# Kernel optimization log

Measured on AMD Instinct MI355X. Metric: run time of the kernel, lower is better.

Reference implementation:

```python
import jax, jax.numpy as jnp
import numpy as np

B, T, F, U = 256, 1024, 64, 128  # batch, history_size, model_input_num, GRU units


def gru(x_seq, W, Uk, b, return_sequences):
    """Keras GRU (reset_after=True, recurrent_activation=sigmoid, activation=relu).
    x_seq: [B,T,F_in]; W: [F_in,3U]; Uk: [U,3U]; b: [2,3U] (input bias, recurrent bias).
    """
    b_i, b_r = b[0], b[1]
    xw = jnp.einsum('bti,iu->btu', x_seq, W) + b_i  # precompute input projection [B,T,3U]

    def step(h, xw_t):
        rec = h @ Uk + b_r                          # [B,3U]
        xz, xr, xh = jnp.split(xw_t, 3, axis=-1)
        rz, rr, rh = jnp.split(rec, 3, axis=-1)
        z = jax.nn.sigmoid(xz + rz)
        r = jax.nn.sigmoid(xr + rr)
        hh = jax.nn.relu(xh + r * rh)
        h_new = z * h + (1.0 - z) * hh
        return h_new, h_new

    h0 = jnp.zeros((x_seq.shape[0], Uk.shape[0]), dtype=x_seq.dtype)
    hT, hs = jax.lax.scan(step, h0, jnp.swapaxes(xw, 0, 1))  # scan over time
    if return_sequences:
        return jnp.swapaxes(hs, 0, 1), hT  # [B,T,U], [B,U]
    return hT, hT


def setup_inputs() -> dict:
    key = jax.random.key(0)
    ks = jax.random.split(key, 7)
    s_in1 = 1.0 / np.sqrt(F)
    s_rec = 1.0 / np.sqrt(U)
    return {
        'input_data': jax.random.normal(ks[0], (B, T, F), dtype=jnp.float32),
        'W1': jax.random.normal(ks[1], (F, 3 * U), dtype=jnp.float32) * s_in1,
        'U1': jax.random.normal(ks[2], (U, 3 * U), dtype=jnp.float32) * s_rec,
        'b1': jnp.zeros((2, 3 * U), dtype=jnp.float32),
        'W2': jax.random.normal(ks[3], (U, 3 * U), dtype=jnp.float32) * s_rec,
        'U2': jax.random.normal(ks[4], (U, 3 * U), dtype=jnp.float32) * s_rec,
        'b2': jnp.zeros((2, 3 * U), dtype=jnp.float32),
    }


def reference(input_data, W1, U1, b1, W2, U2, b2):
    seq1, state1 = gru(input_data, W1, U1, b1, return_sequences=True)
    x, state2 = gru(seq1, W2, U2, b2, return_sequences=False)
    return (x, state1, state2)
```

## Files before the change

### kernel.cpp

```cpp
#include <hip/hip_runtime.h>


#define TT 1024
#define FF 64
#define G3 384
#define NB 16
#define CHUNK 32
#define NCH (TT / CHUNK)
#define FLAG_BYTES ((size_t)NB * NCH * 4)
#define H1F_BYTES ((size_t)NB * TT * 4096)
#define PIPE_WS (FLAG_BYTES + H1F_BYTES)

typedef __attribute__((ext_vector_type(8))) __bf16 bf16x8;
typedef __attribute__((ext_vector_type(4))) float f32x4;

#define MFMA(a, b, c) __builtin_amdgcn_mfma_f32_16x16x32_bf16((a), (b), (c), 0, 0, 0)

__device__ __forceinline__ float sigf(float x) {
    return __builtin_amdgcn_rcpf(1.0f + __expf(-x));
}

__device__ __forceinline__ void wait_flag(const unsigned int* f) {
    while (__hip_atomic_load(f, __ATOMIC_ACQUIRE, __HIP_MEMORY_SCOPE_AGENT) == 0u)
        __builtin_amdgcn_s_sleep(1);
}

__global__ __launch_bounds__(512)
__attribute__((amdgpu_waves_per_eu(2, 2)))
void gru_pipe2(
    const float* __restrict__ x,  const float* __restrict__ W1,
    const float* __restrict__ U1, const float* __restrict__ b1,
    const float* __restrict__ W2, const float* __restrict__ U2,
    const float* __restrict__ b2, unsigned char* __restrict__ ws,
    float* __restrict__ out)
{
    const int tid  = threadIdx.x;
    const int wave = tid >> 6;
    const int lane = tid & 63;
    const int quad = lane >> 4;
    const int lc   = lane & 15;
    const int rb   = blockIdx.x & 15;
    const int row0 = rb * 16;
    const int u    = wave * 16 + lc;

    unsigned int* flags = (unsigned int*)ws + rb * NCH;
    unsigned char* h1f  = ws + FLAG_BYTES + (size_t)rb * TT * 4096;

    __shared__ __align__(16) __bf16 hs[2][16][140];
    for (int i = tid; i < 2 * 16 * 140; i += 512)
        ((__bf16*)hs)[i] = (__bf16)0.f;

    const f32x4 zeroq = {0.f, 0.f, 0.f, 0.f};

    if (blockIdx.x < NB) {
        bf16x8 U1B[3][4], W1B[3][2];
#pragma unroll
        for (int g = 0; g < 3; g++) {
#pragma unroll
            for (int kt = 0; kt < 4; kt++) {
                bf16x8 a;
#pragma unroll
                for (int j = 0; j < 8; j++)
                    a[j] = (__bf16)U1[(kt * 32 + quad * 8 + j) * G3 + g * 128 + u];
                U1B[g][kt] = a;
            }
#pragma unroll
            for (int kt = 0; kt < 2; kt++) {
                bf16x8 a;
#pragma unroll
                for (int j = 0; j < 8; j++)
                    a[j] = (__bf16)W1[(kt * 32 + quad * 8 + j) * G3 + g * 128 + u];
                W1B[g][kt] = a;
            }
        }
        const float c1z  = b1[u] + b1[G3 + u];
        const float c1r  = b1[128 + u] + b1[G3 + 128 + u];
        const float b1ih = b1[256 + u];
        const float b1rh = b1[G3 + 256 + u];
        const f32x4 c1zq  = {c1z, c1z, c1z, c1z};
        const f32x4 c1rq  = {c1r, c1r, c1r, c1r};
        const f32x4 b1ihq = {b1ih, b1ih, b1ih, b1ih};
        const f32x4 b1rhq = {b1rh, b1rh, b1rh, b1rh};

        const float* xrow = x + (size_t)(row0 + lc) * (TT * FF) + quad * 8;
        f32x4 xp0 = *(const f32x4*)(xrow);
        f32x4 xp1 = *(const f32x4*)(xrow + 4);
        f32x4 xp2 = *(const f32x4*)(xrow + 32);
        f32x4 xp3 = *(const f32x4*)(xrow + 36);

        float h1c[4] = {0, 0, 0, 0};
        __syncthreads();

#define PSTEP(T, PAR)                                                          \
    {                                                                          \
        bf16x8 A1[4];                                                          \
        _Pragma("unroll") for (int kt = 0; kt < 4; kt++)                       \
            A1[kt] = *(const bf16x8*)&hs[PAR ^ 1][lc][kt * 32 + quad * 8];     \
        bf16x8 xa0, xa1;                                                       \
        _Pragma("unroll") for (int j = 0; j < 4; j++) {                        \
            xa0[j] = (__bf16)xp0[j]; xa0[j + 4] = (__bf16)xp1[j];              \
            xa1[j] = (__bf16)xp2[j]; xa1[j + 4] = (__bf16)xp3[j];              \
        }                                                                      \
        if ((T) + 1 < TT) {                                                    \
            const float* px = xrow + (size_t)((T) + 1) * FF;                   \
            xp0 = *(const f32x4*)px;                                           \
            xp1 = *(const f32x4*)(px + 4);                                     \
            xp2 = *(const f32x4*)(px + 32);                                    \
            xp3 = *(const f32x4*)(px + 36);                                    \
        }                                                                      \
                    \
        f32x4 z1a = MFMA(xa0, W1B[0][0], c1zq);                                \
        f32x4 r1a = MFMA(xa0, W1B[1][0], c1rq);                                \
        f32x4 xh1 = MFMA(xa0, W1B[2][0], b1ihq);                               \
        z1a = MFMA(xa1, W1B[0][1], z1a);                                       \
        r1a = MFMA(xa1, W1B[1][1], r1a);                                       \
        xh1 = MFMA(xa1, W1B[2][1], xh1);                                       \
                                     \
        f32x4 z1b = MFMA(A1[0], U1B[0][0], zeroq);                             \
        f32x4 r1b = MFMA(A1[0], U1B[1][0], zeroq);                             \
        f32x4 rh1 = MFMA(A1[0], U1B[2][0], b1rhq);                             \
        f32x4 z1d = MFMA(A1[1], U1B[0][1], zeroq);                             \
        f32x4 r1d = MFMA(A1[1], U1B[1][1], zeroq);                             \
        rh1 = MFMA(A1[1], U1B[2][1], rh1);                                     \
        z1b = MFMA(A1[2], U1B[0][2], z1b);                                     \
        r1b = MFMA(A1[2], U1B[1][2], r1b);                                     \
        rh1 = MFMA(A1[2], U1B[2][2], rh1);                                     \
        z1d = MFMA(A1[3], U1B[0][3], z1d);                                     \
        r1d = MFMA(A1[3], U1B[1][3], r1d);                                     \
        rh1 = MFMA(A1[3], U1B[2][3], rh1);                                     \
        if ((T) > 0 && wave == 0) {        \
            _Pragma("unroll") for (int kt = 0; kt < 4; kt++)                   \
                *(bf16x8*)(h1f + ((size_t)((T) - 1) * 4 + kt) * 1024           \
                           + lane * 16) = A1[kt];                              \
        }                                                                      \
        f32x4 z1 = z1a + (z1b + z1d);                                          \
        f32x4 r1 = r1a + (r1b + r1d);                                          \
        _Pragma("unroll") for (int i = 0; i < 4; i++) {                        \
            float zf = sigf(z1[i]);                                            \
            float rf = sigf(r1[i]);                                            \
            float hh = fmaxf(xh1[i] + rf * rh1[i], 0.f);                       \
            h1c[i] = fmaf(zf, h1c[i] - hh, hh);                                \
            hs[PAR][quad * 4 + i][u] = (__bf16)h1c[i];                         \
        }                                                                      \
        if (wave == 0 && (T) > 0 && (((T) & (CHUNK - 1)) == 0)) {              \
            __threadfence();                                                   \
            if (lane == 0)                                                     \
                __hip_atomic_store(flags + ((T) / CHUNK) - 1, 1u,              \
                                   __ATOMIC_RELEASE,                           \
                                   __HIP_MEMORY_SCOPE_AGENT);                  \
        }                                                                      \
        asm volatile("s_waitcnt lgkmcnt(0)\n\ts_barrier" ::: "memory");        \
    }

        for (int t = 0; t < TT; t += 2) {
            PSTEP(t, 0)
            PSTEP(t + 1, 1)
        }
#undef PSTEP

        if (wave == 0) {
#pragma unroll
            for (int kt = 0; kt < 4; kt++) {
                bf16x8 a = *(const bf16x8*)&hs[1][lc][kt * 32 + quad * 8];
                *(bf16x8*)(h1f + ((size_t)(TT - 1) * 4 + kt) * 1024
                           + lane * 16) = a;
            }
            __threadfence();
            if (lane == 0)
                __hip_atomic_store(flags + NCH - 1, 1u, __ATOMIC_RELEASE,
                                   __HIP_MEMORY_SCOPE_AGENT);
        }
#pragma unroll
        for (int i = 0; i < 4; i++) {
            int r = row0 + quad * 4 + i;
            out[32768 + (size_t)r * 128 + u] = h1c[i];
        }
    } else {
        bf16x8 W2B[3][4], U2B[3][4];
#pragma unroll
        for (int g = 0; g < 3; g++)
#pragma unroll
            for (int kt = 0; kt < 4; kt++) {
                bf16x8 b, c;
#pragma unroll
                for (int j = 0; j < 8; j++) {
                    int k = (kt * 32 + quad * 8 + j) * G3 + g * 128 + u;
                    b[j] = (__bf16)W2[k];
                    c[j] = (__bf16)U2[k];
                }
                W2B[g][kt] = b;
                U2B[g][kt] = c;
            }
        const float c2z  = b2[u] + b2[G3 + u];
        const float c2r  = b2[128 + u] + b2[G3 + 128 + u];
        const float b2ih = b2[256 + u];
        const float b2rh = b2[G3 + 256 + u];
        const f32x4 c2zq  = {c2z, c2z, c2z, c2z};
        const f32x4 c2rq  = {c2r, c2r, c2r, c2r};
        const f32x4 b2ihq = {b2ih, b2ih, b2ih, b2ih};
        const f32x4 b2rhq = {b2rh, b2rh, b2rh, b2rh};

        float h2c[4] = {0, 0, 0, 0};
        bf16x8 hAa0, hAa1, hAa2, hAa3, hAb0, hAb1, hAb2, hAb3;
        __syncthreads();

#define CSTEP(T, PAR, C0, C1, C2, C3)                                          \
    {                                                                          \
        bf16x8 A2[4];                                                          \
        _Pragma("unroll") for (int kt = 0; kt < 4; kt++)                       \
            A2[kt] = *(const bf16x8*)&hs[PAR ^ 1][lc][kt * 32 + quad * 8];     \
                    \
        f32x4 z2a = MFMA(C0, W2B[0][0], c2zq);                                 \
        f32x4 r2a = MFMA(C0, W2B[1][0], c2rq);                                 \
        f32x4 xh2 = MFMA(C0, W2B[2][0], b2ihq);                                \
        f32x4 z2c = MFMA(C1, W2B[0][1], zeroq);                                \
        f32x4 r2c = MFMA(C1, W2B[1][1], zeroq);                                \
        xh2 = MFMA(C1, W2B[2][1], xh2);                                        \
        z2a = MFMA(C2, W2B[0][2], z2a);                                        \
        r2a = MFMA(C2, W2B[1][2], r2a);                                        \
        xh2 = MFMA(C2, W2B[2][2], xh2);                                        \
        z2c = MFMA(C3, W2B[0][3], z2c);                                        \
        r2c = MFMA(C3, W2B[1][3], r2c);                                        \
        xh2 = MFMA(C3, W2B[2][3], xh2);                                        \
        if ((T) + 2 < tend) {      \
            const unsigned char* sp =                                          \
                h1f + (size_t)((T) + 2) * 4096 + lane * 16;                    \
            C0 = *(const bf16x8*)(sp);                                         \
            C1 = *(const bf16x8*)(sp + 1024);                                  \
            C2 = *(const bf16x8*)(sp + 2048);                                  \
            C3 = *(const bf16x8*)(sp + 3072);                                  \
        }                                                                      \
                                     \
        f32x4 z2b = MFMA(A2[0], U2B[0][0], zeroq);                             \
        f32x4 r2b = MFMA(A2[0], U2B[1][0], zeroq);                             \
        f32x4 rh2 = MFMA(A2[0], U2B[2][0], b2rhq);                             \
        f32x4 z2d = MFMA(A2[1], U2B[0][1], zeroq);                             \
        f32x4 r2d = MFMA(A2[1], U2B[1][1], zeroq);                             \
        rh2 = MFMA(A2[1], U2B[2][1], rh2);                                     \
        z2b = MFMA(A2[2], U2B[0][2], z2b);                                     \
        r2b = MFMA(A2[2], U2B[1][2], r2b);                                     \
        rh2 = MFMA(A2[2], U2B[2][2], rh2);                                     \
        z2d = MFMA(A2[3], U2B[0][3], z2d);                                     \
        r2d = MFMA(A2[3], U2B[1][3], r2d);                                     \
        rh2 = MFMA(A2[3], U2B[2][3], rh2);                                     \
        f32x4 z2 = (z2a + z2c) + (z2b + z2d);                                  \
        f32x4 r2 = (r2a + r2c) + (r2b + r2d);                                  \
        _Pragma("unroll") for (int i = 0; i < 4; i++) {                        \
            float zf = sigf(z2[i]);                                            \
            float rf = sigf(r2[i]);                                            \
            float hh = fmaxf(xh2[i] + rf * rh2[i], 0.f);                       \
            h2c[i] = fmaf(zf, h2c[i] - hh, hh);                                \
            hs[PAR][quad * 4 + i][u] = (__bf16)h2c[i];                         \
        }                                                                      \
        asm volatile("s_waitcnt lgkmcnt(0)\n\ts_barrier" ::: "memory");        \
    }

        for (int c = 0; c < NCH; c++) {
            wait_flag(flags + c);
            const int t0   = c * CHUNK;
            const int tend = t0 + CHUNK;
            {
                const unsigned char* sp = h1f + (size_t)t0 * 4096 + lane * 16;
                hAa0 = *(const bf16x8*)(sp);
                hAa1 = *(const bf16x8*)(sp + 1024);
                hAa2 = *(const bf16x8*)(sp + 2048);
                hAa3 = *(const bf16x8*)(sp + 3072);
                const unsigned char* sq = sp + 4096;
                hAb0 = *(const bf16x8*)(sq);
                hAb1 = *(const bf16x8*)(sq + 1024);
                hAb2 = *(const bf16x8*)(sq + 2048);
                hAb3 = *(const bf16x8*)(sq + 3072);
            }
            for (int t = t0; t < tend; t += 2) {
                CSTEP(t, 0, hAa0, hAa1, hAa2, hAa3)
                CSTEP(t + 1, 1, hAb0, hAb1, hAb2, hAb3)
            }
        }
#undef CSTEP

#pragma unroll
        for (int i = 0; i < 4; i++) {
            int r = row0 + quad * 4 + i;
            out[(size_t)r * 128 + u]         = h2c[i];
            out[65536 + (size_t)r * 128 + u] = h2c[i];
        }
    }
}

__global__ __launch_bounds__(512)
__attribute__((amdgpu_waves_per_eu(2, 2)))
void gru_mono(
    const float* __restrict__ x,  const float* __restrict__ W1,
    const float* __restrict__ U1, const float* __restrict__ b1,
    const float* __restrict__ W2, const float* __restrict__ U2,
    const float* __restrict__ b2, float* __restrict__ out)
{
    const int tid  = threadIdx.x;
    const int wave = tid >> 6;
    const int lane = tid & 63;
    const int quad = lane >> 4;
    const int lc   = lane & 15;
    const int row0 = blockIdx.x * 16;
    const int u    = wave * 16 + lc;

    __shared__ __align__(16) __bf16 h1s[2][16][136];
    __shared__ __align__(16) __bf16 h2s[2][16][136];
    for (int i = tid; i < 2 * 16 * 136; i += 512) {
        ((__bf16*)h1s)[i] = (__bf16)0.f;
        ((__bf16*)h2s)[i] = (__bf16)0.f;
    }

    bf16x8 U1B[3][4], W2B[3][4], U2B[3][4], W1B[3][2];
#pragma unroll
    for (int g = 0; g < 3; g++) {
#pragma unroll
        for (int kt = 0; kt < 4; kt++) {
            bf16x8 a, b, c;
#pragma unroll
            for (int j = 0; j < 8; j++) {
                int k = (kt * 32 + quad * 8 + j) * G3 + g * 128 + u;
                a[j] = (__bf16)U1[k];
                b[j] = (__bf16)W2[k];
                c[j] = (__bf16)U2[k];
            }
            U1B[g][kt] = a; W2B[g][kt] = b; U2B[g][kt] = c;
        }
#pragma unroll
        for (int kt = 0; kt < 2; kt++) {
            bf16x8 a;
#pragma unroll
            for (int j = 0; j < 8; j++)
                a[j] = (__bf16)W1[(kt * 32 + quad * 8 + j) * G3 + g * 128 + u];
            W1B[g][kt] = a;
        }
    }

    const float c1z  = b1[u] + b1[G3 + u];
    const float c1r  = b1[128 + u] + b1[G3 + 128 + u];
    const float b1ih = b1[256 + u];
    const float b1rh = b1[G3 + 256 + u];
    const float c2z  = b2[u] + b2[G3 + u];
    const float c2r  = b2[128 + u] + b2[G3 + 128 + u];
    const float b2ih = b2[256 + u];
    const float b2rh = b2[G3 + 256 + u];
    const f32x4 c1zq  = {c1z, c1z, c1z, c1z};
    const f32x4 c1rq  = {c1r, c1r, c1r, c1r};
    const f32x4 b1ihq = {b1ih, b1ih, b1ih, b1ih};
    const f32x4 b1rhq = {b1rh, b1rh, b1rh, b1rh};
    const f32x4 c2zq  = {c2z, c2z, c2z, c2z};
    const f32x4 c2rq  = {c2r, c2r, c2r, c2r};
    const f32x4 b2ihq = {b2ih, b2ih, b2ih, b2ih};
    const f32x4 b2rhq = {b2rh, b2rh, b2rh, b2rh};

    const float* xrow = x + (size_t)(row0 + lc) * (TT * FF) + quad * 8;
    float h1c[4] = {0, 0, 0, 0};
    float h2c[4] = {0, 0, 0, 0};
    __syncthreads();

#define MSTEP(T, PAR)                                                          \
    {                                                                          \
        bf16x8 A1[4];                                                          \
        _Pragma("unroll") for (int kt = 0; kt < 4; kt++)                       \
            A1[kt] = *(const bf16x8*)&h1s[PAR ^ 1][lc][kt * 32 + quad * 8];    \
        const float* px = xrow + (size_t)(T) * FF;                             \
        f32x4 u0 = *(const f32x4*)px;                                          \
        f32x4 u1 = *(const f32x4*)(px + 4);                                    \
        f32x4 u2 = *(const f32x4*)(px + 32);                                   \
        f32x4 u3 = *(const f32x4*)(px + 36);                                   \
        bf16x8 xa0, xa1;                                                       \
        _Pragma("unroll") for (int j = 0; j < 4; j++) {                        \
            xa0[j] = (__bf16)u0[j]; xa0[j + 4] = (__bf16)u1[j];                \
            xa1[j] = (__bf16)u2[j]; xa1[j + 4] = (__bf16)u3[j];                \
        }                                                                      \
        f32x4 z1  = MFMA(xa0, W1B[0][0], c1zq);                                \
        z1        = MFMA(xa1, W1B[0][1], z1);                                  \
        f32x4 r1  = MFMA(xa0, W1B[1][0], c1rq);                                \
        r1        = MFMA(xa1, W1B[1][1], r1);                                  \
        f32x4 xh1 = MFMA(xa0, W1B[2][0], b1ihq);                               \
        xh1       = MFMA(xa1, W1B[2][1], xh1);                                 \
        f32x4 rh1 = MFMA(A1[0], U1B[2][0], b1rhq);                             \
        z1        = MFMA(A1[0], U1B[0][0], z1);                                \
        r1        = MFMA(A1[0], U1B[1][0], r1);                                \
        _Pragma("unroll") for (int kt = 1; kt < 4; kt++) {                     \
            z1  = MFMA(A1[kt], U1B[0][kt], z1);                                \
            r1  = MFMA(A1[kt], U1B[1][kt], r1);                                \
            rh1 = MFMA(A1[kt], U1B[2][kt], rh1);                               \
        }                                                                      \
        _Pragma("unroll") for (int i = 0; i < 4; i++) {                        \
            float zf = sigf(z1[i]);                                            \
            float rf = sigf(r1[i]);                                            \
            float hh = fmaxf(xh1[i] + rf * rh1[i], 0.f);                       \
            h1c[i] = fmaf(zf, h1c[i] - hh, hh);                                \
            h1s[PAR][quad * 4 + i][u] = (__bf16)h1c[i];                        \
        }                                                                      \
        f32x4 z2  = MFMA(A1[0], W2B[0][0], c2zq);                              \
        f32x4 r2  = MFMA(A1[0], W2B[1][0], c2rq);                              \
        f32x4 xh2 = MFMA(A1[0], W2B[2][0], b2ihq);                             \
        _Pragma("unroll") for (int kt = 1; kt < 4; kt++) {                     \
            z2  = MFMA(A1[kt], W2B[0][kt], z2);                                \
            r2  = MFMA(A1[kt], W2B[1][kt], r2);                                \
            xh2 = MFMA(A1[kt], W2B[2][kt], xh2);                               \
        }                                                                      \
        f32x4 rh2;                                                             \
        {                                                                      \
            bf16x8 A2 = *(const bf16x8*)&h2s[PAR][lc][quad * 8];               \
            rh2 = MFMA(A2, U2B[2][0], b2rhq);                                  \
            z2  = MFMA(A2, U2B[0][0], z2);                                     \
            r2  = MFMA(A2, U2B[1][0], r2);                                     \
        }                                                                      \
        _Pragma("unroll") for (int kt = 1; kt < 4; kt++) {                     \
            bf16x8 A2 = *(const bf16x8*)&h2s[PAR][lc][kt * 32 + quad * 8];     \
            z2  = MFMA(A2, U2B[0][kt], z2);                                    \
            r2  = MFMA(A2, U2B[1][kt], r2);                                    \
            rh2 = MFMA(A2, U2B[2][kt], rh2);                                   \
        }                                                                      \
        if ((T) > 0) {                                                         \
            _Pragma("unroll") for (int i = 0; i < 4; i++) {                    \
                float zf = sigf(z2[i]);                                        \
                float rf = sigf(r2[i]);                                        \
                float hh = fmaxf(xh2[i] + rf * rh2[i], 0.f);                   \
                h2c[i] = fmaf(zf, h2c[i] - hh, hh);                            \
            }                                                                  \
        }                                                                      \
        _Pragma("unroll") for (int i = 0; i < 4; i++)                          \
            h2s[PAR ^ 1][quad * 4 + i][u] = (__bf16)h2c[i];                    \
        asm volatile("s_waitcnt lgkmcnt(0)\n\ts_barrier" ::: "memory");        \
    }

    for (int t = 0; t < TT; t += 2) {
        MSTEP(t, 0)
        MSTEP(t + 1, 1)
    }
#undef MSTEP

    {
        f32x4 z2 = c2zq, r2 = c2rq, xh2 = b2ihq, rh2 = b2rhq;
#pragma unroll
        for (int kt = 0; kt < 4; kt++) {
            bf16x8 a1 = *(const bf16x8*)&h1s[1][lc][kt * 32 + quad * 8];
            bf16x8 a2 = *(const bf16x8*)&h2s[0][lc][kt * 32 + quad * 8];
            z2  = MFMA(a1, W2B[0][kt], z2);
            r2  = MFMA(a1, W2B[1][kt], r2);
            xh2 = MFMA(a1, W2B[2][kt], xh2);
            z2  = MFMA(a2, U2B[0][kt], z2);
            r2  = MFMA(a2, U2B[1][kt], r2);
            rh2 = MFMA(a2, U2B[2][kt], rh2);
        }
#pragma unroll
        for (int i = 0; i < 4; i++) {
            float zf = sigf(z2[i]);
            float rf = sigf(r2[i]);
            float hh = fmaxf(xh2[i] + rf * rh2[i], 0.f);
            h2c[i] = fmaf(zf, h2c[i] - hh, hh);
        }
    }

#pragma unroll
    for (int i = 0; i < 4; i++) {
        int r = row0 + quad * 4 + i;
        out[(size_t)r * 128 + u]         = h2c[i];
        out[32768 + (size_t)r * 128 + u] = h1c[i];
        out[65536 + (size_t)r * 128 + u] = h2c[i];
    }
}

extern "C" void kernel_launch(void* const* d_in, const int* in_sizes, int n_in,
                              void* d_out, int out_size, void* d_ws, size_t ws_size,
                              hipStream_t stream) {
    const float* x  = (const float*)d_in[0];
    const float* W1 = (const float*)d_in[1];
    const float* U1 = (const float*)d_in[2];
    const float* b1 = (const float*)d_in[3];
    const float* W2 = (const float*)d_in[4];
    const float* U2 = (const float*)d_in[5];
    const float* b2 = (const float*)d_in[6];
    float* out = (float*)d_out;

    if (ws_size >= PIPE_WS) {
        hipMemsetAsync(d_ws, 0, FLAG_BYTES, stream);
        gru_pipe2<<<dim3(2 * NB), dim3(512), 0, stream>>>(
            x, W1, U1, b1, W2, U2, b2, (unsigned char*)d_ws, out);
    } else {
        gru_mono<<<dim3(NB), dim3(512), 0, stream>>>(
            x, W1, U1, b1, W2, U2, b2, out);
    }
}
```

Measured before the change: 1.069 ms.

## Split layer-2 input projection into a separate pipeline stage with ring buffer

Adds a third block role that computes layer 2's input projection (h1·W2) per chunk and writes bf16-packed gate preactivations into a ring buffer in workspace. The layer-2 recurrent blocks then do only the U2 matmul per step, which shortens the serial critical path. Flow control between stages uses flags plus an acknowledgement counter that bounds the ring window. The cost is more workspace traffic, extra bf16 rounding of the preactivations, and added inter-block synchronisation. It also needs 48 co-resident blocks.

Measured after the change: 1.172 ms. 1.1x slower.

```diff
diff --git a/kernel.cpp b/kernel.cpp
--- a/kernel.cpp
+++ b/kernel.cpp
@@ -7,9 +7,12 @@
 #define NB 16
 #define CHUNK 32
 #define NCH (TT / CHUNK)
-#define FLAG_BYTES ((size_t)NB * NCH * 4)
+#define XWINC 16
+#define XMASK (XWINC * CHUNK - 1)
+#define FLAGS_TOTAL 8192
 #define H1F_BYTES ((size_t)NB * TT * 4096)
-#define PIPE_WS (FLAG_BYTES + H1F_BYTES)
+#define XW2_BYTES ((size_t)(XWINC * CHUNK) * NB * 12288)
+#define PIPE_WS (FLAGS_TOTAL + H1F_BYTES + XW2_BYTES)
 
 typedef __attribute__((ext_vector_type(8))) __bf16 bf16x8;
 typedef __attribute__((ext_vector_type(4))) float f32x4;
@@ -18,6 +21,15 @@
 
 __device__ __forceinline__ float sigf(float x) {
     return __builtin_amdgcn_rcpf(1.0f + __expf(-x));
+}
+
+__device__ __forceinline__ f32x4 unpackv(uint2 v) {
+    f32x4 o;
+    o[0] = __uint_as_float(v.x << 16);
+    o[1] = __uint_as_float(v.x & 0xFFFF0000u);
+    o[2] = __uint_as_float(v.y << 16);
+    o[3] = __uint_as_float(v.y & 0xFFFF0000u);
+    return o;
 }
 
 __device__ __forceinline__ void wait_flag(const unsigned int* f) {
@@ -27,7 +39,7 @@
 
 __global__ __launch_bounds__(512)
 __attribute__((amdgpu_waves_per_eu(2, 2)))
-void gru_pipe2(
+void gru_pipe3(
     const float* __restrict__ x,  const float* __restrict__ W1,
     const float* __restrict__ U1, const float* __restrict__ b1,
     const float* __restrict__ W2, const float* __restrict__ U2,
@@ -39,20 +51,26 @@
     const int lane = tid & 63;
     const int quad = lane >> 4;
     const int lc   = lane & 15;
+    const int role = blockIdx.x >> 4;
     const int rb   = blockIdx.x & 15;
     const int row0 = rb * 16;
     const int u    = wave * 16 + lc;
 
-    unsigned int* flags = (unsigned int*)ws + rb * NCH;
-    unsigned char* h1f  = ws + FLAG_BYTES + (size_t)rb * TT * 4096;
+    unsigned int* flag1 = (unsigned int*)ws + rb * NCH;
+    unsigned int* flag2 = (unsigned int*)(ws + 2048) + rb * NCH;
+    unsigned int* uackp = (unsigned int*)(ws + 4096) + rb;
+    unsigned char* h1f  = ws + FLAGS_TOTAL + (size_t)rb * TT * 4096;
+    uint2* xw2 = (uint2*)(ws + FLAGS_TOTAL + H1F_BYTES);
 
     __shared__ __align__(16) __bf16 hs[2][16][140];
-    for (int i = tid; i < 2 * 16 * 140; i += 512)
-        ((__bf16*)hs)[i] = (__bf16)0.f;
+    if (role != 1) {
+        for (int i = tid; i < 2 * 16 * 140; i += 512)
+            ((__bf16*)hs)[i] = (__bf16)0.f;
+    }
 
     const f32x4 zeroq = {0.f, 0.f, 0.f, 0.f};
 
-    if (blockIdx.x < NB) {
+    if (role == 0) {
         bf16x8 U1B[3][4], W1B[3][2];
 #pragma unroll
         for (int g = 0; g < 3; g++) {
@@ -108,14 +126,12 @@
             xp2 = *(const f32x4*)(px + 32);                                    \
             xp3 = *(const f32x4*)(px + 36);                                    \
         }                                                                      \
-                    \
         f32x4 z1a = MFMA(xa0, W1B[0][0], c1zq);                                \
         f32x4 r1a = MFMA(xa0, W1B[1][0], c1rq);                                \
         f32x4 xh1 = MFMA(xa0, W1B[2][0], b1ihq);                               \
         z1a = MFMA(xa1, W1B[0][1], z1a);                                       \
         r1a = MFMA(xa1, W1B[1][1], r1a);                                       \
         xh1 = MFMA(xa1, W1B[2][1], xh1);                                       \
-                                     \
         f32x4 z1b = MFMA(A1[0], U1B[0][0], zeroq);                             \
         f32x4 r1b = MFMA(A1[0], U1B[1][0], zeroq);                             \
         f32x4 rh1 = MFMA(A1[0], U1B[2][0], b1rhq);                             \
@@ -128,7 +144,7 @@
         z1d = MFMA(A1[3], U1B[0][3], z1d);                                     \
         r1d = MFMA(A1[3], U1B[1][3], r1d);                                     \
         rh1 = MFMA(A1[3], U1B[2][3], rh1);                                     \
-        if ((T) > 0 && wave == 0) {        \
+        if ((T) > 0 && wave == 0) {                                            \
             _Pragma("unroll") for (int kt = 0; kt < 4; kt++)                   \
                 *(bf16x8*)(h1f + ((size_t)((T) - 1) * 4 + kt) * 1024           \
                            + lane * 16) = A1[kt];                              \
@@ -145,7 +161,7 @@
         if (wave == 0 && (T) > 0 && (((T) & (CHUNK - 1)) == 0)) {              \
             __threadfence();                                                   \
             if (lane == 0)                                                     \
-                __hip_atomic_store(flags + ((T) / CHUNK) - 1, 1u,              \
+                __hip_atomic_store(flag1 + ((T) / CHUNK) - 1, 1u,              \
                                    __ATOMIC_RELEASE,                           \
                                    __HIP_MEMORY_SCOPE_AGENT);                  \
         }                                                                      \
@@ -167,7 +183,7 @@
             }
             __threadfence();
             if (lane == 0)
-                __hip_atomic_store(flags + NCH - 1, 1u, __ATOMIC_RELEASE,
+                __hip_atomic_store(flag1 + NCH - 1, 1u, __ATOMIC_RELEASE,
                                    __HIP_MEMORY_SCOPE_AGENT);
         }
 #pragma unroll
@@ -175,76 +191,132 @@
             int r = row0 + quad * 4 + i;
             out[32768 + (size_t)r * 128 + u] = h1c[i];
         }
-    } else {
-        bf16x8 W2B[3][4], U2B[3][4];
+    } else if (role == 1) {
+        bf16x8 W2B[3][4];
 #pragma unroll
         for (int g = 0; g < 3; g++)
 #pragma unroll
             for (int kt = 0; kt < 4; kt++) {
-                bf16x8 b, c;
-#pragma unroll
-                for (int j = 0; j < 8; j++) {
-                    int k = (kt * 32 + quad * 8 + j) * G3 + g * 128 + u;
-                    b[j] = (__bf16)W2[k];
-                    c[j] = (__bf16)U2[k];
-                }
+                bf16x8 b;
+#pragma unroll
+                for (int j = 0; j < 8; j++)
+                    b[j] = (__bf16)W2[(kt * 32 + quad * 8 + j) * G3 + g * 128 + u];
                 W2B[g][kt] = b;
-                U2B[g][kt] = c;
             }
         const float c2z  = b2[u] + b2[G3 + u];
         const float c2r  = b2[128 + u] + b2[G3 + 128 + u];
         const float b2ih = b2[256 + u];
-        const float b2rh = b2[G3 + 256 + u];
         const f32x4 c2zq  = {c2z, c2z, c2z, c2z};
         const f32x4 c2rq  = {c2r, c2r, c2r, c2r};
         const f32x4 b2ihq = {b2ih, b2ih, b2ih, b2ih};
+
+        bf16x8 Aa0, Aa1, Aa2, Aa3, Ab0, Ab1, Ab2, Ab3;
+
+#define WSTEP(T, C0, C1, C2, C3, N0, N1, N2, N3)                               \
+    {                                                                          \
+        if ((T) + 1 < tend) {                                                  \
+            const unsigned char* sp =                                          \
+                h1f + (size_t)((T) + 1) * 4096 + lane * 16;                    \
+            N0 = *(const bf16x8*)(sp);                                         \
+            N1 = *(const bf16x8*)(sp + 1024);                                  \
+            N2 = *(const bf16x8*)(sp + 2048);                                  \
+            N3 = *(const bf16x8*)(sp + 3072);                                  \
+        }                                                                      \
+        f32x4 z = MFMA(C0, W2B[0][0], c2zq);                                   \
+        f32x4 r = MFMA(C0, W2B[1][0], c2rq);                                   \
+        f32x4 h = MFMA(C0, W2B[2][0], b2ihq);                                  \
+        z = MFMA(C1, W2B[0][1], z);                                            \
+        r = MFMA(C1, W2B[1][1], r);                                            \
+        h = MFMA(C1, W2B[2][1], h);                                            \
+        z = MFMA(C2, W2B[0][2], z);                                            \
+        r = MFMA(C2, W2B[1][2], r);                                            \
+        h = MFMA(C2, W2B[2][2], h);                                            \
+        z = MFMA(C3, W2B[0][3], z);                                            \
+        r = MFMA(C3, W2B[1][3], r);                                            \
+        h = MFMA(C3, W2B[2][3], h);                                            \
+        uint2* xq = xw2 + (((size_t)((T) & XMASK) * 16 + rb) * 3) * 512        \
+                    + wave * 64 + lane;                                        \
+        f32x4 gv[3] = {z, r, h};                                               \
+        _Pragma("unroll") for (int g = 0; g < 3; g++) {                        \
+            unsigned int s0 = __builtin_bit_cast(unsigned short, (__bf16)gv[g][0]); \
+            unsigned int s1 = __builtin_bit_cast(unsigned short, (__bf16)gv[g][1]); \
+            unsigned int s2 = __builtin_bit_cast(unsigned short, (__bf16)gv[g][2]); \
+            unsigned int s3 = __builtin_bit_cast(unsigned short, (__bf16)gv[g][3]); \
+            uint2 st;                                                          \
+            st.x = s0 | (s1 << 16);                                            \
+            st.y = s2 | (s3 << 16);                                            \
+            xq[(size_t)g * 512] = st;                                          \
+        }                                                                      \
+    }
+
+        for (int c = 0; c < NCH; c++) {
+            wait_flag(flag1 + c);
+            if (c >= XWINC) {
+                while ((int)__hip_atomic_load(uackp, __ATOMIC_ACQUIRE,
+                                              __HIP_MEMORY_SCOPE_AGENT)
+                       < c - XWINC + 1)
+                    __builtin_amdgcn_s_sleep(1);
+            }
+            const int t0   = c * CHUNK;
+            const int tend = t0 + CHUNK;
+            {
+                const unsigned char* sp = h1f + (size_t)t0 * 4096 + lane * 16;
+                Aa0 = *(const bf16x8*)(sp);
+                Aa1 = *(const bf16x8*)(sp + 1024);
+                Aa2 = *(const bf16x8*)(sp + 2048);
+                Aa3 = *(const bf16x8*)(sp + 3072);
+            }
+            for (int t = t0; t < tend; t += 2) {
+                WSTEP(t, Aa0, Aa1, Aa2, Aa3, Ab0, Ab1, Ab2, Ab3)
+                WSTEP(t + 1, Ab0, Ab1, Ab2, Ab3, Aa0, Aa1, Aa2, Aa3)
+            }
+            __threadfence();
+            __syncthreads();
+            if (tid == 0)
+                __hip_atomic_store(flag2 + c, 1u, __ATOMIC_RELEASE,
+                                   __HIP_MEMORY_SCOPE_AGENT);
+        }
+#undef WSTEP
+    } else {
+        bf16x8 U2B[3][4];
+#pragma unroll
+        for (int g = 0; g < 3; g++)
+#pragma unroll
+            for (int kt = 0; kt < 4; kt++) {
+                bf16x8 cfr;
+#pragma unroll
+                for (int j = 0; j < 8; j++)
+                    cfr[j] = (__bf16)U2[(kt * 32 + quad * 8 + j) * G3 + g * 128 + u];
+                U2B[g][kt] = cfr;
+            }
+        const float b2rh = b2[G3 + 256 + u];
         const f32x4 b2rhq = {b2rh, b2rh, b2rh, b2rh};
 
+        const uint2* xqb = xw2 + (size_t)rb * 1536 + wave * 64 + lane;
+        uint2 xwv[3];
         float h2c[4] = {0, 0, 0, 0};
-        bf16x8 hAa0, hAa1, hAa2, hAa3, hAb0, hAb1, hAb2, hAb3;
         __syncthreads();
 
-#define CSTEP(T, PAR, C0, C1, C2, C3)                                          \
+#define USTEP(T, PAR)                                                          \
     {                                                                          \
+        f32x4 z2  = unpackv(xwv[0]);                                           \
+        f32x4 r2  = unpackv(xwv[1]);                                           \
+        f32x4 xh2 = unpackv(xwv[2]);                                           \
+        if ((T) + 1 < tend) {                                                  \
+            _Pragma("unroll") for (int g = 0; g < 3; g++)                      \
+                xwv[g] = xqb[(size_t)(((T) + 1) & XMASK) * 24576 + g * 512];   \
+        }                                                                      \
         bf16x8 A2[4];                                                          \
         _Pragma("unroll") for (int kt = 0; kt < 4; kt++)                       \
             A2[kt] = *(const bf16x8*)&hs[PAR ^ 1][lc][kt * 32 + quad * 8];     \
-                    \
-        f32x4 z2a = MFMA(C0, W2B[0][0], c2zq);                                 \
-        f32x4 r2a = MFMA(C0, W2B[1][0], c2rq);                                 \
-        f32x4 xh2 = MFMA(C0, W2B[2][0], b2ihq);                                \
-        f32x4 z2c = MFMA(C1, W2B[0][1], zeroq);                                \
-        f32x4 r2c = MFMA(C1, W2B[1][1], zeroq);                                \
-        xh2 = MFMA(C1, W2B[2][1], xh2);                                        \
-        z2a = MFMA(C2, W2B[0][2], z2a);                                        \
-        r2a = MFMA(C2, W2B[1][2], r2a);                                        \
-        xh2 = MFMA(C2, W2B[2][2], xh2);                                        \
-        z2c = MFMA(C3, W2B[0][3], z2c);                                        \
-        r2c = MFMA(C3, W2B[1][3], r2c);                                        \
-        xh2 = MFMA(C3, W2B[2][3], xh2);                                        \
-        if ((T) + 2 < tend) {      \
-            const unsigned char* sp =                                          \
-                h1f + (size_t)((T) + 2) * 4096 + lane * 16;                    \
-            C0 = *(const bf16x8*)(sp);                                         \
-            C1 = *(const bf16x8*)(sp + 1024);                                  \
-            C2 = *(const bf16x8*)(sp + 2048);                                  \
-            C3 = *(const bf16x8*)(sp + 3072);                                  \
-        }                                                                      \
-                                     \
-        f32x4 z2b = MFMA(A2[0], U2B[0][0], zeroq);                             \
-        f32x4 r2b = MFMA(A2[0], U2B[1][0], zeroq);                             \
         f32x4 rh2 = MFMA(A2[0], U2B[2][0], b2rhq);                             \
-        f32x4 z2d = MFMA(A2[1], U2B[0][1], zeroq);                             \
-        f32x4 r2d = MFMA(A2[1], U2B[1][1], zeroq);                             \
-        rh2 = MFMA(A2[1], U2B[2][1], rh2);                                     \
-        z2b = MFMA(A2[2], U2B[0][2], z2b);                                     \
-        r2b = MFMA(A2[2], U2B[1][2], r2b);                                     \
-        rh2 = MFMA(A2[2], U2B[2][2], rh2);                                     \
-        z2d = MFMA(A2[3], U2B[0][3], z2d);                                     \
-        r2d = MFMA(A2[3], U2B[1][3], r2d);                                     \
-        rh2 = MFMA(A2[3], U2B[2][3], rh2);                                     \
-        f32x4 z2 = (z2a + z2c) + (z2b + z2d);                                  \
-        f32x4 r2 = (r2a + r2c) + (r2b + r2d);                                  \
+        z2 = MFMA(A2[0], U2B[0][0], z2);                                       \
+        r2 = MFMA(A2[0], U2B[1][0], r2);                                       \
+        _Pragma("unroll") for (int kt = 1; kt < 4; kt++) {                     \
+            z2  = MFMA(A2[kt], U2B[0][kt], z2);                                \
+            r2  = MFMA(A2[kt], U2B[1][kt], r2);                                \
+            rh2 = MFMA(A2[kt], U2B[2][kt], rh2);                               \
+        }                                                                      \
         _Pragma("unroll") for (int i = 0; i < 4; i++) {                        \
             float zf = sigf(z2[i]);                                            \
             float rf = sigf(r2[i]);                                            \
@@ -256,27 +328,21 @@
     }
 
         for (int c = 0; c < NCH; c++) {
-            wait_flag(flags + c);
+            wait_flag(flag2 + c);
             const int t0   = c * CHUNK;
             const int tend = t0 + CHUNK;
-            {
-                const unsigned char* sp = h1f + (size_t)t0 * 4096 + lane * 16;
-                hAa0 = *(const bf16x8*)(sp);
-                hAa1 = *(const bf16x8*)(sp + 1024);
-                hAa2 = *(const bf16x8*)(sp + 2048);
-                hAa3 = *(const bf16x8*)(sp + 3072);
-                const unsigned char* sq = sp + 4096;
-                hAb0 = *(const bf16x8*)(sq);
-                hAb1 = *(const bf16x8*)(sq + 1024);
-                hAb2 = *(const bf16x8*)(sq + 2048);
-                hAb3 = *(const bf16x8*)(sq + 3072);
-            }
+#pragma unroll
+            for (int g = 0; g < 3; g++)
+                xwv[g] = xqb[(size_t)(t0 & XMASK) * 24576 + g * 512];
             for (int t = t0; t < tend; t += 2) {
-                CSTEP(t, 0, hAa0, hAa1, hAa2, hAa3)
-                CSTEP(t + 1, 1, hAb0, hAb1, hAb2, hAb3)
-            }
-        }
-#undef CSTEP
+                USTEP(t, 0)
+                USTEP(t + 1, 1)
+            }
+            if (tid == 0)
+                __hip_atomic_store(uackp, (unsigned int)(c + 1),
+                                   __ATOMIC_RELEASE, __HIP_MEMORY_SCOPE_AGENT);
+        }
+#undef USTEP
 
 #pragma unroll
         for (int i = 0; i < 4; i++) {
@@ -303,9 +369,9 @@
     const int row0 = blockIdx.x * 16;
     const int u    = wave * 16 + lc;
 
-    __shared__ __align__(16) __bf16 h1s[2][16][136];
-    __shared__ __align__(16) __bf16 h2s[2][16][136];
-    for (int i = tid; i < 2 * 16 * 136; i += 512) {
+    __shared__ __align__(16) __bf16 h1s[2][16][140];
+    __shared__ __align__(16) __bf16 h2s[2][16][140];
+    for (int i = tid; i < 2 * 16 * 140; i += 512) {
         ((__bf16*)h1s)[i] = (__bf16)0.f;
         ((__bf16*)h2s)[i] = (__bf16)0.f;
     }
@@ -477,8 +543,8 @@
     float* out = (float*)d_out;
 
     if (ws_size >= PIPE_WS) {
-        hipMemsetAsync(d_ws, 0, FLAG_BYTES, stream);
-        gru_pipe2<<<dim3(2 * NB), dim3(512), 0, stream>>>(
+        hipMemsetAsync(d_ws, 0, FLAGS_TOTAL, stream);
+        gru_pipe3<<<dim3(3 * NB), dim3(512), 0, stream>>>(
             x, W1, U1, b1, W2, U2, b2, (unsigned char*)d_ws, out);
     } else {
         gru_mono<<<dim3(NB), dim3(512), 0, stream>>>(
```
